# Kernel optimization log

Hardware: AMD Instinct MI355X
Metric: run time of the kernel (lower is better)

Reference implementation:

```python
import jax, jax.numpy as jnp
import numpy as np

E, W, C, D, F = 8, 8, 1024, 512, 2048  # local experts, world_size, capacity, d_model, d_ff


def setup_inputs() -> dict:
    key = jax.random.key(0)
    k1, k2, k3 = jax.random.split(key, 3)
    x = jax.random.normal(k1, (E, W, C, D), dtype=jnp.float32)
    cap = jax.random.randint(jax.random.fold_in(key, 7), (E,), 0, C)
    wi = jax.random.normal(k2, (E, D, F), dtype=jnp.float32) * 0.02
    wo = jax.random.normal(k3, (E, F, D), dtype=jnp.float32) * 0.02
    return {
        "dispatched_hidden_states": x,
        "experts_capacity_usage": cap,
        "wi": wi,
        "wo": wo,
    }


def reference(dispatched_hidden_states, experts_capacity_usage, wi, wo):
    # LocalExperts (handle_by_capacity=False): each expert e applies its own
    # T5 FFN to its chunk x[e]; expressed as a grouped GEMM over the expert axis.
    h = jnp.einsum("ewcd,edf->ewcf", dispatched_hidden_states, wi)  # [E,W,C,F]
    h = jax.nn.relu(h)
    out = jnp.einsum("ewcf,efd->ewcd", h, wo)  # [E,W,C,D]
    return out
```

## Files before the change

kernel.cpp:

```cpp
#include <hip/hip_runtime.h>
#include <hip/hip_bf16.h>
#include <stdint.h>


#define E_N 8
#define W_N 8
#define C_N 1024
#define D_N 512
#define F_N 2048
#define ME  (W_N * C_N)

typedef __attribute__((ext_vector_type(4))) float f32x4;
typedef __attribute__((ext_vector_type(8))) short s16x8;

#define BAR()  __builtin_amdgcn_s_barrier()
#define SBAR() __builtin_amdgcn_sched_barrier(0)
#define CFENCE() do { asm volatile("" ::: "memory"); SBAR(); } while (0)
#define LGKM0() do { asm volatile("s_waitcnt lgkmcnt(0)" ::: "memory"); SBAR(); } while (0)
#define VM8()   do { asm volatile("s_waitcnt vmcnt(8)"   ::: "memory"); SBAR(); } while (0)
#define VM0()   do { asm volatile("s_waitcnt vmcnt(0)"   ::: "memory"); SBAR(); } while (0)

__device__ __forceinline__ unsigned short f2bf(float f) {
  union { float f; unsigned int u; } v; v.f = f;
  unsigned int u = v.u + 0x7fffu + ((v.u >> 16) & 1u);
  return (unsigned short)(u >> 16);
}

__device__ __forceinline__ void gload_lds16(void* lds, const void* g) {
  __builtin_amdgcn_global_load_lds(
      (const __attribute__((address_space(1))) unsigned int*)g,
      (__attribute__((address_space(3))) unsigned int*)lds, 16, 0, 0);
}

__device__ __forceinline__ void transpose_tile(
    const float* __restrict__ in, unsigned short* __restrict__ out,
    int R, int Ccols, int bx, int by, int bz) {
  __shared__ unsigned short tile[64][65];
  const float* ip = in + (size_t)bz * R * Ccols;
  unsigned short* op = out + (size_t)bz * R * Ccols;
  const int c0 = bx * 64, r0 = by * 64;
  const int t = threadIdx.x;
  const int cl = (t & 15) * 4, rw = t >> 4;
#pragma unroll
  for (int i = 0; i < 4; ++i) {
    int row = rw + i * 16;
    float4 v = *(const float4*)&ip[(size_t)(r0 + row) * Ccols + c0 + cl];
    tile[row][cl + 0] = f2bf(v.x);
    tile[row][cl + 1] = f2bf(v.y);
    tile[row][cl + 2] = f2bf(v.z);
    tile[row][cl + 3] = f2bf(v.w);
  }
  __syncthreads();
#pragma unroll
  for (int i = 0; i < 4; ++i) {
    int oc = rw + i * 16;
    ushort4 o;
    o.x = tile[cl + 0][oc];
    o.y = tile[cl + 1][oc];
    o.z = tile[cl + 2][oc];
    o.w = tile[cl + 3][oc];
    *(ushort4*)&op[(size_t)(c0 + oc) * R + r0 + cl] = o;
  }
}

__global__ __launch_bounds__(256)
void prep_fused(const float* __restrict__ x, const float* __restrict__ wi,
                const float* __restrict__ wo, unsigned short* __restrict__ xb,
                unsigned short* __restrict__ wiT, unsigned short* __restrict__ woT) {
  const int id = blockIdx.x;
  if (id < 2048) {
    transpose_tile(wi, wiT, D_N, F_N, id % 32, (id / 32) % 8, id / 256);
  } else if (id < 4096) {
    const int v = id - 2048;
    transpose_tile(wo, woT, F_N, D_N, v % 8, (v / 8) % 32, v / 256);
  } else {
    const int v = id - 4096;
    const size_t n = (size_t)E_N * ME * D_N;
    size_t idx = ((size_t)v * 256 + threadIdx.x) * 8;
    const size_t stride = (size_t)2048 * 256 * 8;
    for (; idx < n; idx += stride) {
      float4 a = *(const float4*)&x[idx];
      float4 b = *(const float4*)&x[idx + 4];
      union { s16x8 v8; unsigned short u[8]; } p;
      p.u[0] = f2bf(a.x); p.u[1] = f2bf(a.y); p.u[2] = f2bf(a.z); p.u[3] = f2bf(a.w);
      p.u[4] = f2bf(b.x); p.u[5] = f2bf(b.y); p.u[6] = f2bf(b.z); p.u[7] = f2bf(b.w);
      *(s16x8*)&xb[idx] = p.v8;
    }
  }
}

template<bool RELU_BF16_OUT>
__global__ __launch_bounds__(512, 2)
void gemm256p(const unsigned short* __restrict__ Abase,
              const unsigned short* __restrict__ Btbase,
              void* __restrict__ Cv, int N, int K, int nT,
              size_t aStrideE, size_t bStrideE, size_t cStrideE) {
  extern __shared__ unsigned short lds[];
  unsigned char* ldsb = (unsigned char*)lds;
  const int blk = blockIdx.x;
  const int e  = blk & 7;
  const int bi = blk >> 3;
  const int TS = nT;
  const int n0 = (bi % nT) * 256;
  const int ms = bi / nT;
  const int tid  = threadIdx.x;
  const int lane = tid & 63;
  const int wave = tid >> 6;
  const int wm = wave >> 2;
  const int wn = wave & 3;
  const unsigned short* A  = Abase  + (size_t)e * aStrideE;
  const unsigned short* Bt = Btbase + (size_t)e * bStrideE;

  const int NK = K >> 6;
  const int kshift = __builtin_ctz(NK);
  const int total = TS * NK;

  const int rl = lane & 15;
  const int gb = lane >> 4;
  const int g16_0 = ((0 * 4 + gb) ^ (rl & 7)) * 16;
  const int g16_1 = ((1 * 4 + gb) ^ (rl & 7)) * 16;
  const int aBase0 = wm * 16384 + rl * 128;
  const int bBase0 = 32768 + (wn >> 1) * 16384 + ((wn & 1) * 64 + rl) * 128;

  int rA0[2], rB0[2];
#pragma unroll
  for (int o = 0; o < 2; ++o) {
    int G = o * 512 + tid;
    int r = G >> 3;
    int gl = (G & 7) ^ (r & 7);
    rA0[o] = r * K + gl * 8;
    rB0[o] = (n0 + r) * K + gl * 8;
  }
  auto stageA = [&](int g, int h) {
    const int ktl = g & (NK - 1);
    const int buf = g & 1;
    const int m0t = (ms * TS + (g >> kshift)) * 256;
    const unsigned short* An = A + (size_t)m0t * K;
#pragma unroll
    for (int o = 0; o < 2; ++o)
      gload_lds16(ldsb + buf * 65536 + h * 16384 + o * 8192 + wave * 1024,
                  An + rA0[o] + h * 128 * K + ktl * 64);
  };
  auto stageB = [&](int g, int h) {
    const int ktl = g & (NK - 1);
    const int buf = g & 1;
#pragma unroll
    for (int o = 0; o < 2; ++o)
      gload_lds16(ldsb + buf * 65536 + 32768 + h * 16384 + o * 8192 + wave * 1024,
                  Bt + rB0[o] + h * 128 * K + ktl * 64);
  };

  f32x4 acc[8][4] = {};

  auto run_ktile = [&](int buf, int gN, bool more, bool needDrain) {
    const int bufOff = buf * 65536;
    s16x8 afr[4][2], b01[2][2], b23[2][2];
#pragma unroll
    for (int mi = 0; mi < 4; ++mi) {
      afr[mi][0] = *(const s16x8*)(ldsb + bufOff + aBase0 + mi * 2048 + g16_0);
      afr[mi][1] = *(const s16x8*)(ldsb + bufOff + aBase0 + mi * 2048 + g16_1);
    }
#pragma unroll
    for (int ni = 0; ni < 2; ++ni) {
      b01[ni][0] = *(const s16x8*)(ldsb + bufOff + bBase0 + ni * 2048 + g16_0);
      b01[ni][1] = *(const s16x8*)(ldsb + bufOff + bBase0 + ni * 2048 + g16_1);
    }
    BAR(); LGKM0();
    __builtin_amdgcn_s_setprio(1);
#pragma unroll
    for (int mi = 0; mi < 4; ++mi)
#pragma unroll
      for (int ni = 0; ni < 2; ++ni) {
        acc[mi][ni] = __builtin_amdgcn_mfma_f32_16x16x32_bf16(afr[mi][0], b01[ni][0], acc[mi][ni], 0, 0, 0);
        acc[mi][ni] = __builtin_amdgcn_mfma_f32_16x16x32_bf16(afr[mi][1], b01[ni][1], acc[mi][ni], 0, 0, 0);
      }
    __builtin_amdgcn_s_setprio(0);
    BAR();
#pragma unroll
    for (int ni = 0; ni < 2; ++ni) {
      b23[ni][0] = *(const s16x8*)(ldsb + bufOff + bBase0 + (2 + ni) * 2048 + g16_0);
      b23[ni][1] = *(const s16x8*)(ldsb + bufOff + bBase0 + (2 + ni) * 2048 + g16_1);
    }
    BAR(); LGKM0();
    __builtin_amdgcn_s_setprio(1);
#pragma unroll
    for (int mi = 0; mi < 4; ++mi)
#pragma unroll
      for (int ni = 0; ni < 2; ++ni) {
        acc[mi][2 + ni] = __builtin_amdgcn_mfma_f32_16x16x32_bf16(afr[mi][0], b23[ni][0], acc[mi][2 + ni], 0, 0, 0);
        acc[mi][2 + ni] = __builtin_amdgcn_mfma_f32_16x16x32_bf16(afr[mi][1], b23[ni][1], acc[mi][2 + ni], 0, 0, 0);
      }
    __builtin_amdgcn_s_setprio(0);
    BAR();
#pragma unroll
    for (int mi = 0; mi < 4; ++mi) {
      afr[mi][0] = *(const s16x8*)(ldsb + bufOff + aBase0 + (4 + mi) * 2048 + g16_0);
      afr[mi][1] = *(const s16x8*)(ldsb + bufOff + aBase0 + (4 + mi) * 2048 + g16_1);
    }
    if (more) { stageB(gN, 0); stageB(gN, 1); }
    BAR(); LGKM0();
    __builtin_amdgcn_s_setprio(1);
#pragma unroll
    for (int mi = 0; mi < 4; ++mi)
#pragma unroll
      for (int ni = 0; ni < 2; ++ni) {
        acc[4 + mi][2 + ni] = __builtin_amdgcn_mfma_f32_16x16x32_bf16(afr[mi][0], b23[ni][0], acc[4 + mi][2 + ni], 0, 0, 0);
        acc[4 + mi][2 + ni] = __builtin_amdgcn_mfma_f32_16x16x32_bf16(afr[mi][1], b23[ni][1], acc[4 + mi][2 + ni], 0, 0, 0);
      }
    __builtin_amdgcn_s_setprio(0);
    BAR();
    if (more) { stageA(gN, 0); stageA(gN, 1); }
    BAR();
    __builtin_amdgcn_s_setprio(1);
#pragma unroll
    for (int mi = 0; mi < 4; ++mi)
#pragma unroll
      for (int ni = 0; ni < 2; ++ni) {
        acc[4 + mi][ni] = __builtin_amdgcn_mfma_f32_16x16x32_bf16(afr[mi][0], b01[ni][0], acc[4 + mi][ni], 0, 0, 0);
        acc[4 + mi][ni] = __builtin_amdgcn_mfma_f32_16x16x32_bf16(afr[mi][1], b01[ni][1], acc[4 + mi][ni], 0, 0, 0);
      }
    __builtin_amdgcn_s_setprio(0);
    if (more) { VM8(); } else if (needDrain) { VM0(); }
    BAR();
  };

  stageB(0, 0); stageB(0, 1); stageA(0, 0); stageA(0, 1);
  stageB(1, 0); stageB(1, 1); stageA(1, 0); stageA(1, 1);
  VM8();
  BAR();

  const int rq = (lane >> 4) * 4;
  const int cq = lane & 15;
  unsigned short* slabW = (unsigned short*)(ldsb + 131072) + wave * (16 * 66);
  const int r_rd = lane >> 2;
  const int c_rd = (lane & 3) * 16;

  for (int g = 0; g < total; g += 2) {
    run_ktile(0, g + 2, (g + 2 < total), true);
    run_ktile(1, g + 3, (g + 3 < total), false);
    if (((g + 2) & (NK - 1)) == 0) {
      const int m0 = (ms * TS + (g >> kshift)) * 256;
      if (RELU_BF16_OUT) {
        unsigned short* Cb = (unsigned short*)Cv + (size_t)e * cStrideE;
#pragma unroll
        for (int mi = 0; mi < 8; ++mi) {
#pragma unroll
          for (int ni = 0; ni < 4; ++ni)
#pragma unroll
            for (int r = 0; r < 4; ++r) {
              float v = acc[mi][ni][r];
              v = v > 0.f ? v : 0.f;
              slabW[(rq + r) * 66 + ni * 16 + cq] = f2bf(v);
            }
          LGKM0();
          uint4 w0 = *(const uint4*)&slabW[r_rd * 66 + c_rd];
          uint4 w1 = *(const uint4*)&slabW[r_rd * 66 + c_rd + 8];
          unsigned short* dst =
              Cb + (size_t)(m0 + wm * 128 + mi * 16 + r_rd) * N + n0 + wn * 64 + c_rd;
          *(uint4*)dst = w0;
          *(uint4*)(dst + 8) = w1;
        }
        CFENCE();
      } else {
        float* Cf = (float*)Cv + (size_t)e * cStrideE;
#pragma unroll
        for (int mi = 0; mi < 8; ++mi)
#pragma unroll
          for (int ni = 0; ni < 4; ++ni) {
            int row0 = m0 + wm * 128 + mi * 16 + rq;
            int col  = n0 + wn * 64 + ni * 16 + cq;
#pragma unroll
            for (int r = 0; r < 4; ++r)
              Cf[(size_t)(row0 + r) * N + col] = acc[mi][ni][r];
          }
      }
#pragma unroll
      for (int mi = 0; mi < 8; ++mi)
#pragma unroll
        for (int ni = 0; ni < 4; ++ni)
          acc[mi][ni] = (f32x4){0.f, 0.f, 0.f, 0.f};
    }
  }
}

__global__ __launch_bounds__(256)
void fused_naive(const float* __restrict__ x, const float* __restrict__ wi,
                 const float* __restrict__ wo, float* __restrict__ out) {
  __shared__ float xs[D_N];
  __shared__ float hs[F_N];
  const size_t row = blockIdx.x;
  const int e = (int)(row / (W_N * C_N));
  const float* xr = x + row * D_N;
  const float* wie = wi + (size_t)e * D_N * F_N;
  const float* woe = wo + (size_t)e * F_N * D_N;
  const int t = threadIdx.x;
  for (int d = t; d < D_N; d += 256) xs[d] = xr[d];
  __syncthreads();
  for (int f = t; f < F_N; f += 256) {
    float a = 0.f;
    for (int d = 0; d < D_N; ++d) a += xs[d] * wie[(size_t)d * F_N + f];
    hs[f] = a > 0.f ? a : 0.f;
  }
  __syncthreads();
  float* orow = out + row * D_N;
  for (int d = t; d < D_N; d += 256) {
    float a = 0.f;
    for (int f = 0; f < F_N; ++f) a += hs[f] * woe[(size_t)f * D_N + d];
    orow[d] = a;
  }
}

extern "C" void kernel_launch(void* const* d_in, const int* in_sizes, int n_in,
                              void* d_out, int out_size, void* d_ws, size_t ws_size,
                              hipStream_t stream) {
  const float* x  = (const float*)d_in[0];
  const float* wi = (const float*)d_in[2];
  const float* wo = (const float*)d_in[3];
  float* out = (float*)d_out;

  const size_t WT   = (size_t)E_N * D_N * F_N;
  unsigned short* wiT = (unsigned short*)d_ws;
  unsigned short* woT = wiT + WT;
  unsigned short* P   = woT + WT;
  const size_t baseB = 2 * WT * 2;
  const size_t XB_B  = (size_t)E_N * ME * D_N * 2;
  const size_t HF_B  = (size_t)E_N * ME * F_N * 2;

  const dim3 blk(256);
  if (ws_size >= baseB + XB_B + HF_B) {
    hipFuncSetAttribute(reinterpret_cast<const void*>(gemm256p<true>),
                        hipFuncAttributeMaxDynamicSharedMemorySize, 147968);
    hipFuncSetAttribute(reinterpret_cast<const void*>(gemm256p<false>),
                        hipFuncAttributeMaxDynamicSharedMemorySize, 131072);
    unsigned short* xb = P;
    unsigned short* h  = P + XB_B / 2;
    prep_fused<<<dim3(6144), blk, 0, stream>>>(x, wi, wo, xb, wiT, woT);
    gemm256p<true><<<dim3(256), dim3(512), 147968, stream>>>(
        xb, wiT, h, F_N, D_N, F_N / 256,
        (size_t)ME * D_N, (size_t)F_N * D_N, (size_t)ME * F_N);
    gemm256p<false><<<dim3(256), dim3(512), 131072, stream>>>(
        h, woT, out, D_N, F_N, D_N / 256,
        (size_t)ME * F_N, (size_t)D_N * F_N, (size_t)ME * D_N);
  } else {
    fused_naive<<<dim3(E_N * W_N * C_N), blk, 0, stream>>>(x, wi, wo, out);
  }
}
```

Baseline: 364.4 us.

## Stage fp32 epilogue through LDS with nontemporal vector stores and adjust waits

The fp32 output epilogue of the second GEMM now goes through a per-wave LDS slab, so each row is written with 16-byte coalesced nontemporal stores instead of scattered scalar stores. The bf16 epilogue also switches to nontemporal stores. Because the epilogue's global stores now add to the outstanding vmcnt, the first k-tile after an epilogue waits with a larger vmcnt threshold. The second GEMM's dynamic LDS grows to hold the slab, and the epilogue adds extra LDS round trips and barriers.

Result: faster. 337.3 us, median of 2 (-7.4%).

```diff
diff --git a/kernel.cpp b/kernel.cpp
--- a/kernel.cpp
+++ b/kernel.cpp
@@ -11,6 +11,7 @@
 #define ME  (W_N * C_N)
 
 typedef __attribute__((ext_vector_type(4))) float f32x4;
+typedef __attribute__((ext_vector_type(4))) unsigned int u32x4;
 typedef __attribute__((ext_vector_type(8))) short s16x8;
 
 #define BAR()  __builtin_amdgcn_s_barrier()
@@ -18,6 +19,8 @@
 #define CFENCE() do { asm volatile("" ::: "memory"); SBAR(); } while (0)
 #define LGKM0() do { asm volatile("s_waitcnt lgkmcnt(0)" ::: "memory"); SBAR(); } while (0)
 #define VM8()   do { asm volatile("s_waitcnt vmcnt(8)"   ::: "memory"); SBAR(); } while (0)
+#define VM24()  do { asm volatile("s_waitcnt vmcnt(24)"  ::: "memory"); SBAR(); } while (0)
+#define VM40()  do { asm volatile("s_waitcnt vmcnt(40)"  ::: "memory"); SBAR(); } while (0)
 #define VM0()   do { asm volatile("s_waitcnt vmcnt(0)"   ::: "memory"); SBAR(); } while (0)
 
 __device__ __forceinline__ unsigned short f2bf(float f) {
@@ -152,7 +155,7 @@
 
   f32x4 acc[8][4] = {};
 
-  auto run_ktile = [&](int buf, int gN, bool more, bool needDrain) {
+  auto run_ktile = [&](int buf, int gN, bool more, bool needDrain, bool bigWait) {
     const int bufOff = buf * 65536;
     s16x8 afr[4][2], b01[2][2], b23[2][2];
 #pragma unroll
@@ -220,7 +223,10 @@
         acc[4 + mi][ni] = __builtin_amdgcn_mfma_f32_16x16x32_bf16(afr[mi][1], b01[ni][1], acc[4 + mi][ni], 0, 0, 0);
       }
     __builtin_amdgcn_s_setprio(0);
-    if (more) { VM8(); } else if (needDrain) { VM0(); }
+    if (more) {
+      if (bigWait) { if (RELU_BF16_OUT) { VM24(); } else { VM40(); } }
+      else         { VM8(); }
+    } else if (needDrain) { VM0(); }
     BAR();
   };
 
@@ -231,13 +237,17 @@
 
   const int rq = (lane >> 4) * 4;
   const int cq = lane & 15;
-  unsigned short* slabW = (unsigned short*)(ldsb + 131072) + wave * (16 * 66);
+  unsigned short* slabW = (unsigned short*)(ldsb + 131072) + wave * 1056;
+  float*          slabF = (float*)(ldsb + 131072) + wave * 528;
   const int r_rd = lane >> 2;
   const int c_rd = (lane & 3) * 16;
+  const int fr_rd = lane >> 3;
+  const int fc_rd = (lane & 7) * 4;
 
   for (int g = 0; g < total; g += 2) {
-    run_ktile(0, g + 2, (g + 2 < total), true);
-    run_ktile(1, g + 3, (g + 3 < total), false);
+    const bool bigW = (g > 0) && ((g & (NK - 1)) == 0);
+    run_ktile(0, g + 2, (g + 2 < total), true, bigW);
+    run_ktile(1, g + 3, (g + 3 < total), false, false);
     if (((g + 2) & (NK - 1)) == 0) {
       const int m0 = (ms * TS + (g >> kshift)) * 256;
       if (RELU_BF16_OUT) {
@@ -253,26 +263,37 @@
               slabW[(rq + r) * 66 + ni * 16 + cq] = f2bf(v);
             }
           LGKM0();
-          uint4 w0 = *(const uint4*)&slabW[r_rd * 66 + c_rd];
-          uint4 w1 = *(const uint4*)&slabW[r_rd * 66 + c_rd + 8];
+          u32x4 w0 = *(const u32x4*)&slabW[r_rd * 66 + c_rd];
+          u32x4 w1 = *(const u32x4*)&slabW[r_rd * 66 + c_rd + 8];
           unsigned short* dst =
               Cb + (size_t)(m0 + wm * 128 + mi * 16 + r_rd) * N + n0 + wn * 64 + c_rd;
-          *(uint4*)dst = w0;
-          *(uint4*)(dst + 8) = w1;
+          __builtin_nontemporal_store(w0, (u32x4*)dst);
+          __builtin_nontemporal_store(w1, (u32x4*)(dst + 8));
         }
         CFENCE();
       } else {
         float* Cf = (float*)Cv + (size_t)e * cStrideE;
 #pragma unroll
-        for (int mi = 0; mi < 8; ++mi)
-#pragma unroll
-          for (int ni = 0; ni < 4; ++ni) {
-            int row0 = m0 + wm * 128 + mi * 16 + rq;
-            int col  = n0 + wn * 64 + ni * 16 + cq;
-#pragma unroll
-            for (int r = 0; r < 4; ++r)
-              Cf[(size_t)(row0 + r) * N + col] = acc[mi][ni][r];
+        for (int mi = 0; mi < 8; ++mi) {
+#pragma unroll
+          for (int hr = 0; hr < 2; ++hr) {
+            if ((rq >> 3) == hr) {
+#pragma unroll
+              for (int ni = 0; ni < 4; ++ni)
+#pragma unroll
+                for (int r = 0; r < 4; ++r)
+                  slabF[((rq & 7) + r) * 66 + ni * 16 + cq] = acc[mi][ni][r];
+            }
+            LGKM0();
+            f32x4 w0 = *(const f32x4*)&slabF[fr_rd * 66 + fc_rd];
+            f32x4 w1 = *(const f32x4*)&slabF[fr_rd * 66 + 32 + fc_rd];
+            float* dst =
+                Cf + (size_t)(m0 + wm * 128 + mi * 16 + hr * 8 + fr_rd) * N + n0 + wn * 64;
+            __builtin_nontemporal_store(w0, (f32x4*)(dst + fc_rd));
+            __builtin_nontemporal_store(w1, (f32x4*)(dst + 32 + fc_rd));
           }
+        }
+        CFENCE();
       }
 #pragma unroll
       for (int mi = 0; mi < 8; ++mi)
@@ -331,14 +352,14 @@
     hipFuncSetAttribute(reinterpret_cast<const void*>(gemm256p<true>),
                         hipFuncAttributeMaxDynamicSharedMemorySize, 147968);
     hipFuncSetAttribute(reinterpret_cast<const void*>(gemm256p<false>),
-                        hipFuncAttributeMaxDynamicSharedMemorySize, 131072);
+                        hipFuncAttributeMaxDynamicSharedMemorySize, 147968);
     unsigned short* xb = P;
     unsigned short* h  = P + XB_B / 2;
     prep_fused<<<dim3(6144), blk, 0, stream>>>(x, wi, wo, xb, wiT, woT);
     gemm256p<true><<<dim3(256), dim3(512), 147968, stream>>>(
         xb, wiT, h, F_N, D_N, F_N / 256,
         (size_t)ME * D_N, (size_t)F_N * D_N, (size_t)ME * F_N);
-    gemm256p<false><<<dim3(256), dim3(512), 131072, stream>>>(
+    gemm256p<false><<<dim3(256), dim3(512), 147968, stream>>>(
         h, woT, out, D_N, F_N, D_N / 256,
         (size_t)ME * F_N, (size_t)D_N * F_N, (size_t)ME * D_N);
   } else {
```
